# Performance work log

Measured on AMD Instinct MI355X. Metric: run time of the kernel, lower is better.

## Reference

```python
import jax, jax.numpy as jnp
import numpy as np

IN_CHS = 128
NUM_HEADS = 4
WIN = 7
N = WIN * WIN            # 49 tokens per window
QKDIM = 128              # ceil(in_chs/num_groups/num_heads)*num_heads
HEAD_DIM = QKDIM // NUM_HEADS
SCALE = HEAD_DIM ** -0.5
B = 4096                 # batch * num_windows


def _relative_position_index(win_h, win_w):
    coords = np.stack(np.meshgrid(np.arange(win_h), np.arange(win_w), indexing='ij'))  # [2,h,w]
    cf = coords.reshape(2, -1)                      # [2, N]
    rc = (cf[:, :, None] - cf[:, None, :]).transpose(1, 2, 0).astype(np.int64)  # [N,N,2]
    rc[:, :, 0] += win_h - 1
    rc[:, :, 1] += win_w - 1
    rc[:, :, 0] *= 2 * win_w - 1
    return rc.sum(-1)                               # [N, N]


def setup_inputs() -> dict:
    key = jax.random.key(0)
    ks = jax.random.split(key, 8)
    x = jax.random.normal(ks[0], (B, N, IN_CHS), dtype=jnp.float32)
    qk_w = jax.random.normal(ks[1], (2 * QKDIM, IN_CHS), dtype=jnp.float32) * 0.02
    qk_b = jnp.zeros((2 * QKDIM,), dtype=jnp.float32)
    v_w = jax.random.normal(ks[2], (IN_CHS, IN_CHS), dtype=jnp.float32) * 0.02
    v_b = jnp.zeros((IN_CHS,), dtype=jnp.float32)
    proj_w = jax.random.normal(ks[3], (IN_CHS, IN_CHS), dtype=jnp.float32) * 0.02
    proj_b = jnp.zeros((IN_CHS,), dtype=jnp.float32)
    bias_table = jax.random.normal(ks[4], ((2 * WIN - 1) * (2 * WIN - 1), NUM_HEADS), dtype=jnp.float32) * 0.02
    rel_idx = jnp.asarray(_relative_position_index(WIN, WIN))  # [N,N] int64
    return {"x": x, "qk_w": qk_w, "qk_b": qk_b, "v_w": v_w, "v_b": v_b,
            "proj_w": proj_w, "proj_b": proj_b, "bias_table": bias_table,
            "rel_idx": rel_idx}


def reference(x, qk_w, qk_b, v_w, v_b, proj_w, proj_b, bias_table, rel_idx):
    Bn, Nn, C = x.shape
    # fused q/k projection: [B,N,2*qkdim] -> q,k each [B,H,N,d]
    qk = (x @ qk_w.T + qk_b).reshape(Bn, Nn, 2, NUM_HEADS, HEAD_DIM)
    q = qk[:, :, 0].transpose(0, 2, 1, 3)
    k = qk[:, :, 1].transpose(0, 2, 1, 3)
    v = (x @ v_w.T + v_b).reshape(Bn, Nn, NUM_HEADS, -1).transpose(0, 2, 1, 3)
    # windowed QK^T with gathered relative-position bias
    attn = jnp.einsum('bhnd,bhmd->bhnm', q * SCALE, k)
    bias = bias_table[rel_idx.reshape(-1)].reshape(Nn, Nn, NUM_HEADS).transpose(2, 0, 1)
    attn = jax.nn.softmax(attn + bias[None], axis=-1)
    out = jnp.einsum('bhnm,bhmd->bhnd', attn, v).transpose(0, 2, 1, 3).reshape(Bn, Nn, -1)
    return out @ proj_w.T + proj_b
```

## Files before the change

kernel.cpp:

```cpp
#include <hip/hip_runtime.h>
#include <hip/hip_bf16.h>

typedef __attribute__((ext_vector_type(8))) __bf16 bf16x8;
typedef __attribute__((ext_vector_type(4))) float f32x4;

#define MFMA(a,b,c) __builtin_amdgcn_mfma_f32_16x16x32_bf16((a),(b),(c),0,0,0)

#define XB 0u
#define QB 16384u
#define KB 32768u
#define VT 49152u

static __device__ __forceinline__ unsigned short f2u(float x) {
  return __builtin_bit_cast(unsigned short, static_cast<__bf16>(x));
}
static __device__ __forceinline__ unsigned long long pack4(float a, float b, float c, float d) {
  return (unsigned long long)f2u(a) | ((unsigned long long)f2u(b) << 16) |
         ((unsigned long long)f2u(c) << 32) | ((unsigned long long)f2u(d) << 48);
}
static __device__ __forceinline__ unsigned sw256(unsigned row, unsigned colb) {
  return (row << 8) + (colb ^ ((row & 7u) << 4));
}
static __device__ __forceinline__ unsigned sw128(unsigned row, unsigned colb) {
  return (row << 7) + (colb ^ ((row & 7u) << 4));
}

__global__ void rsa_prep(const float* __restrict__ qk_w, const float* __restrict__ v_w,
                         const float* __restrict__ proj_w, const float* __restrict__ bias_table,
                         unsigned short* __restrict__ wqk, unsigned short* __restrict__ wv,
                         unsigned short* __restrict__ wp, float* __restrict__ biasNN) {
  int t = blockIdx.x * blockDim.x + threadIdx.x;
  int stride = gridDim.x * blockDim.x;
  for (int i = t; i < 256 * 128; i += stride) wqk[i] = f2u(qk_w[i]);
  for (int i = t; i < 128 * 128; i += stride) wv[i] = f2u(v_w[i]);
  for (int i = t; i < 128 * 128; i += stride) wp[i] = f2u(proj_w[i]);
  for (int i = t; i < 4 * 64 * 64; i += stride) {
    int h = i >> 12, r = (i >> 6) & 63, m = i & 63;
    float v = -1e9f;
    if (r < 49 && m < 49) {
      int ri = r / 7, rj = r - ri * 7, mi = m / 7, mj = m - mi * 7;
      int rel = (ri - mi + 6) * 13 + (rj - mj + 6);
      v = bias_table[rel * 4 + h];
    }
    biasNN[i] = v;
  }
}

__global__ __launch_bounds__(512, 4) void rsa_main(
    const float* __restrict__ x, const float* __restrict__ qk_bias,
    const float* __restrict__ v_bias, const float* __restrict__ proj_bias,
    const unsigned short* __restrict__ wqk, const unsigned short* __restrict__ wv,
    const unsigned short* __restrict__ wp, const float* __restrict__ biasNN,
    float* __restrict__ out) {
  __shared__ __align__(16) unsigned char LDS[65536];
  const int tid = threadIdx.x;
  const int w = tid >> 6;
  const int lane = tid & 63;
  const int c = lane & 15;
  const int g = lane >> 4;
  const int b = blockIdx.x;
  const float SCALE = 0.17677669529663687f;

  {
    const f32x4* xp = reinterpret_cast<const f32x4*>(x + (size_t)b * 6272);
    for (int i = tid; i < 1568; i += 512) {
      f32x4 v = xp[i];
      unsigned row = (unsigned)i >> 5, c4 = (unsigned)i & 31;
      *reinterpret_cast<unsigned long long*>(LDS + XB + sw256(row, c4 * 8)) =
          pack4(v[0], v[1], v[2], v[3]);
    }
    for (int i = tid; i < 480; i += 512) {
      unsigned row = 49 + ((unsigned)i >> 5), c4 = (unsigned)i & 31;
      *reinterpret_cast<unsigned long long*>(LDS + XB + sw256(row, c4 * 8)) = 0ull;
    }
  }
  __syncthreads();

#pragma unroll
  for (int mi = 0; mi < 2; ++mi) {
    const int mt = w + 8 * mi;
    bf16x8 a[4];
    const unsigned short* wrow = wqk + (mt * 16 + c) * 128 + g * 8;
#pragma unroll
    for (int ks = 0; ks < 4; ++ks) a[ks] = *reinterpret_cast<const bf16x8*>(wrow + ks * 32);
    const int chout = mt * 16 + g * 4;
    f32x4 bias4 = *reinterpret_cast<const f32x4*>(qk_bias + chout);
#pragma unroll
    for (int nt = 0; nt < 4; ++nt) {
      f32x4 acc = {0.f, 0.f, 0.f, 0.f};
#pragma unroll
      for (int ks = 0; ks < 4; ++ks) {
        bf16x8 bf = *reinterpret_cast<const bf16x8*>(LDS + XB + sw256(nt * 16 + c, (ks * 32 + g * 8) * 2));
        acc = MFMA(a[ks], bf, acc);
      }
      const unsigned tok = nt * 16 + c;
      const unsigned colb = ((mt & 7) * 16 + g * 4) * 2;
      float v0 = acc[0] + bias4[0], v1 = acc[1] + bias4[1];
      float v2 = acc[2] + bias4[2], v3 = acc[3] + bias4[3];
      if (mi == 0) { v0 *= SCALE; v1 *= SCALE; v2 *= SCALE; v3 *= SCALE; }
      const unsigned base = (mi == 0) ? QB : KB;
      *reinterpret_cast<unsigned long long*>(LDS + base + sw256(tok, colb)) = pack4(v0, v1, v2, v3);
    }
  }

  {
    const float vb = v_bias[w * 16 + c];
    bf16x8 bw[4];
    const unsigned short* wrow = wv + (w * 16 + c) * 128 + g * 8;
#pragma unroll
    for (int ks = 0; ks < 4; ++ks) bw[ks] = *reinterpret_cast<const bf16x8*>(wrow + ks * 32);
#pragma unroll
    for (int mt = 0; mt < 4; ++mt) {
      f32x4 acc = {0.f, 0.f, 0.f, 0.f};
#pragma unroll
      for (int ks = 0; ks < 4; ++ks) {
        bf16x8 af = *reinterpret_cast<const bf16x8*>(LDS + XB + sw256(mt * 16 + c, (ks * 32 + g * 8) * 2));
        acc = MFMA(af, bw[ks], acc);
      }
      const unsigned row = w * 16 + c;
      const unsigned colb = (mt * 16 + g * 4) * 2;
      *reinterpret_cast<unsigned long long*>(LDS + VT + sw128(row, colb)) =
          pack4(acc[0] + vb, acc[1] + vb, acc[2] + vb, acc[3] + vb);
    }
  }
  __syncthreads();

  const int h = w >> 1;
  const int rt0 = (w & 1) * 2;
  f32x4 s[2][4];
#pragma unroll
  for (int r2 = 0; r2 < 2; ++r2) {
    const int rt = rt0 + r2;
    bf16x8 qf = *reinterpret_cast<const bf16x8*>(LDS + QB + sw256(rt * 16 + c, h * 64 + g * 16));
#pragma unroll
    for (int mt = 0; mt < 4; ++mt) {
      bf16x8 kf = *reinterpret_cast<const bf16x8*>(LDS + KB + sw256(mt * 16 + c, h * 64 + g * 16));
      f32x4 z = {0.f, 0.f, 0.f, 0.f};
      s[r2][mt] = MFMA(kf, qf, z);
    }
  }
  __syncthreads();

#pragma unroll
  for (int r2 = 0; r2 < 2; ++r2) {
    const int r = (rt0 + r2) * 16 + c;
    const float* bp = biasNN + ((h * 64 + r) << 6);
    float v[16];
#pragma unroll
    for (int mt = 0; mt < 4; ++mt) {
      f32x4 bb = *reinterpret_cast<const f32x4*>(bp + mt * 16 + g * 4);
#pragma unroll
      for (int j = 0; j < 4; ++j) v[mt * 4 + j] = s[r2][mt][j] + bb[j];
    }
    float mx = v[0];
#pragma unroll
    for (int j = 1; j < 16; ++j) mx = fmaxf(mx, v[j]);
    mx = fmaxf(mx, __shfl_xor(mx, 16));
    mx = fmaxf(mx, __shfl_xor(mx, 32));
    float sum = 0.f;
#pragma unroll
    for (int j = 0; j < 16; ++j) { v[j] = __expf(v[j] - mx); sum += v[j]; }
    sum += __shfl_xor(sum, 16);
    sum += __shfl_xor(sum, 32);
    const float inv = 1.0f / sum;
#pragma unroll
    for (int mt = 0; mt < 4; ++mt) {
      *reinterpret_cast<unsigned long long*>(LDS + QB + h * 8192 + sw128(r, (mt * 16 + g * 4) * 2)) =
          pack4(v[mt * 4] * inv, v[mt * 4 + 1] * inv, v[mt * 4 + 2] * inv, v[mt * 4 + 3] * inv);
    }
  }

#pragma unroll
  for (int dt = 0; dt < 2; ++dt) {
#pragma unroll
    for (int r2 = 0; r2 < 2; ++r2) {
      const int r = (rt0 + r2) * 16 + c;
      f32x4 acc = {0.f, 0.f, 0.f, 0.f};
#pragma unroll
      for (int ks = 0; ks < 2; ++ks) {
        bf16x8 af = *reinterpret_cast<const bf16x8*>(LDS + VT + sw128(h * 32 + dt * 16 + c, (ks * 32 + g * 8) * 2));
        bf16x8 pf = *reinterpret_cast<const bf16x8*>(LDS + QB + h * 8192 + sw128(r, (ks * 32 + g * 8) * 2));
        acc = MFMA(af, pf, acc);
      }
      const unsigned colb = (h * 32 + dt * 16 + g * 4) * 2;
      *reinterpret_cast<unsigned long long*>(LDS + XB + sw256(r, colb)) =
          pack4(acc[0], acc[1], acc[2], acc[3]);
    }
  }
  __syncthreads();

  {
    bf16x8 ap[4];
    const unsigned short* wrow = wp + (w * 16 + c) * 128 + g * 8;
#pragma unroll
    for (int ks = 0; ks < 4; ++ks) ap[ks] = *reinterpret_cast<const bf16x8*>(wrow + ks * 32);
    f32x4 pb4 = *reinterpret_cast<const f32x4*>(proj_bias + w * 16 + g * 4);
#pragma unroll
    for (int nt = 0; nt < 4; ++nt) {
      f32x4 acc = {0.f, 0.f, 0.f, 0.f};
#pragma unroll
      for (int ks = 0; ks < 4; ++ks) {
        bf16x8 bf = *reinterpret_cast<const bf16x8*>(LDS + XB + sw256(nt * 16 + c, (ks * 32 + g * 8) * 2));
        acc = MFMA(ap[ks], bf, acc);
      }
      const int tok = nt * 16 + c;
      if (tok < 49) {
        f32x4 o = {acc[0] + pb4[0], acc[1] + pb4[1], acc[2] + pb4[2], acc[3] + pb4[3]};
        *reinterpret_cast<f32x4*>(out + ((size_t)b * 49 + tok) * 128 + w * 16 + g * 4) = o;
      }
    }
  }
}

extern "C" void kernel_launch(void* const* d_in, const int* in_sizes, int n_in,
                              void* d_out, int out_size, void* d_ws, size_t ws_size,
                              hipStream_t stream) {
  const float* x          = (const float*)d_in[0];
  const float* qk_w       = (const float*)d_in[1];
  const float* qk_b       = (const float*)d_in[2];
  const float* v_w        = (const float*)d_in[3];
  const float* v_b        = (const float*)d_in[4];
  const float* proj_w     = (const float*)d_in[5];
  const float* proj_b     = (const float*)d_in[6];
  const float* bias_table = (const float*)d_in[7];
  float* out = (float*)d_out;

  unsigned short* wqk = (unsigned short*)d_ws;
  unsigned short* wv  = wqk + 256 * 128;
  unsigned short* wp  = wv + 128 * 128;
  float* biasNN = (float*)((char*)d_ws + 131072);

  const int B = in_sizes[0] / (49 * 128);

  rsa_prep<<<dim3(128), dim3(512), 0, stream>>>(qk_w, v_w, proj_w, bias_table, wqk, wv, wp, biasNN);
  rsa_main<<<dim3(B), dim3(512), 0, stream>>>(x, qk_b, v_b, proj_b, wqk, wv, wp, biasNN, out);
}
```

Before: 126.6 us.

## Process eight windows per block with register-resident weights and x prefetch

Each block now loops over eight windows instead of one. The Q, K and V weight fragments and the biases are loaded into registers once per block. The next window's x tile is prefetched into registers while the current window is being computed. The Q, K and V projections are fused into one loop that shares the x fragments, and the softmax drops the row-max subtraction. This cuts repeated weight loads and block launch overhead, and overlaps global loads with compute. In exchange it raises register pressure under the existing launch bounds, which may cause spills. It also shrinks the grid to 512 blocks, leaving less parallelism to hide latency, and skipping the max subtraction risks overflow for large logits.

After: 213.7 us. +68.8%, slower.

```diff
diff --git a/kernel.cpp b/kernel.cpp
--- a/kernel.cpp
+++ b/kernel.cpp
@@ -10,6 +10,7 @@
 #define QB 16384u
 #define KB 32768u
 #define VT 49152u
+#define NW 8
 
 static __device__ __forceinline__ unsigned short f2u(float x) {
   return __builtin_bit_cast(unsigned short, static_cast<__bf16>(x));
@@ -17,6 +18,9 @@
 static __device__ __forceinline__ unsigned long long pack4(float a, float b, float c, float d) {
   return (unsigned long long)f2u(a) | ((unsigned long long)f2u(b) << 16) |
          ((unsigned long long)f2u(c) << 32) | ((unsigned long long)f2u(d) << 48);
+}
+static __device__ __forceinline__ unsigned long long pack4v(f32x4 v) {
+  return pack4(v[0], v[1], v[2], v[3]);
 }
 static __device__ __forceinline__ unsigned sw256(unsigned row, unsigned colb) {
   return (row << 8) + (colb ^ ((row & 7u) << 4));
@@ -51,164 +55,164 @@
     const float* __restrict__ v_bias, const float* __restrict__ proj_bias,
     const unsigned short* __restrict__ wqk, const unsigned short* __restrict__ wv,
     const unsigned short* __restrict__ wp, const float* __restrict__ biasNN,
-    float* __restrict__ out) {
+    float* __restrict__ out, int Btot) {
   __shared__ __align__(16) unsigned char LDS[65536];
   const int tid = threadIdx.x;
   const int w = tid >> 6;
   const int lane = tid & 63;
   const int c = lane & 15;
   const int g = lane >> 4;
-  const int b = blockIdx.x;
   const float SCALE = 0.17677669529663687f;
 
+  bf16x8 aq[4], ak[4], bv[4];
+  {
+    const unsigned short* rq = wqk + (w * 16 + c) * 128 + g * 8;
+    const unsigned short* rk = wqk + (128 + w * 16 + c) * 128 + g * 8;
+    const unsigned short* rv = wv + (w * 16 + c) * 128 + g * 8;
+#pragma unroll
+    for (int ks = 0; ks < 4; ++ks) {
+      aq[ks] = *reinterpret_cast<const bf16x8*>(rq + ks * 32);
+      ak[ks] = *reinterpret_cast<const bf16x8*>(rk + ks * 32);
+      bv[ks] = *reinterpret_cast<const bf16x8*>(rv + ks * 32);
+    }
+  }
+  const f32x4 qb4 = *reinterpret_cast<const f32x4*>(qk_bias + w * 16 + g * 4);
+  const f32x4 kb4 = *reinterpret_cast<const f32x4*>(qk_bias + 128 + w * 16 + g * 4);
+  const f32x4 pb4 = *reinterpret_cast<const f32x4*>(proj_bias + w * 16 + g * 4);
+  const float vb = v_bias[w * 16 + c];
+  const int h = w >> 1;
+  const int rt0 = (w & 1) * 2;
+
+  int b = blockIdx.x * NW;
+  if (b >= Btot) return;
+  const int nw = (Btot - b < NW) ? (Btot - b) : NW;
+
+  f32x4 xr[4];
   {
     const f32x4* xp = reinterpret_cast<const f32x4*>(x + (size_t)b * 6272);
-    for (int i = tid; i < 1568; i += 512) {
-      f32x4 v = xp[i];
-      unsigned row = (unsigned)i >> 5, c4 = (unsigned)i & 31;
-      *reinterpret_cast<unsigned long long*>(LDS + XB + sw256(row, c4 * 8)) =
-          pack4(v[0], v[1], v[2], v[3]);
-    }
-    for (int i = tid; i < 480; i += 512) {
-      unsigned row = 49 + ((unsigned)i >> 5), c4 = (unsigned)i & 31;
-      *reinterpret_cast<unsigned long long*>(LDS + XB + sw256(row, c4 * 8)) = 0ull;
-    }
-  }
-  __syncthreads();
-
-#pragma unroll
-  for (int mi = 0; mi < 2; ++mi) {
-    const int mt = w + 8 * mi;
-    bf16x8 a[4];
-    const unsigned short* wrow = wqk + (mt * 16 + c) * 128 + g * 8;
-#pragma unroll
-    for (int ks = 0; ks < 4; ++ks) a[ks] = *reinterpret_cast<const bf16x8*>(wrow + ks * 32);
-    const int chout = mt * 16 + g * 4;
-    f32x4 bias4 = *reinterpret_cast<const f32x4*>(qk_bias + chout);
+#pragma unroll
+    for (int j = 0; j < 3; ++j) xr[j] = xp[tid + j * 512];
+    if (tid < 32) xr[3] = xp[tid + 1536];
+    else xr[3] = f32x4{0.f, 0.f, 0.f, 0.f};
+  }
+
+  for (int i = 0; i < nw; ++i) {
+#pragma unroll
+    for (int j = 0; j < 4; ++j) {
+      unsigned idx = (unsigned)tid + (unsigned)j * 512u;
+      unsigned row = idx >> 5, c4 = idx & 31u;
+      *reinterpret_cast<unsigned long long*>(LDS + XB + sw256(row, c4 * 8)) = pack4v(xr[j]);
+    }
+    __syncthreads();
+
+    if (i + 1 < nw) {
+      const f32x4* xp = reinterpret_cast<const f32x4*>(x + (size_t)(b + 1) * 6272);
+#pragma unroll
+      for (int j = 0; j < 3; ++j) xr[j] = xp[tid + j * 512];
+      if (tid < 32) xr[3] = xp[tid + 1536];
+    }
+
 #pragma unroll
     for (int nt = 0; nt < 4; ++nt) {
-      f32x4 acc = {0.f, 0.f, 0.f, 0.f};
+      bf16x8 xf[4];
+#pragma unroll
+      for (int ks = 0; ks < 4; ++ks)
+        xf[ks] = *reinterpret_cast<const bf16x8*>(LDS + XB + sw256(nt * 16 + c, (ks * 32 + g * 8) * 2));
+      f32x4 accq = {0.f, 0.f, 0.f, 0.f}, acck = {0.f, 0.f, 0.f, 0.f}, accv = {0.f, 0.f, 0.f, 0.f};
 #pragma unroll
       for (int ks = 0; ks < 4; ++ks) {
-        bf16x8 bf = *reinterpret_cast<const bf16x8*>(LDS + XB + sw256(nt * 16 + c, (ks * 32 + g * 8) * 2));
-        acc = MFMA(a[ks], bf, acc);
+        accq = MFMA(aq[ks], xf[ks], accq);
+        acck = MFMA(ak[ks], xf[ks], acck);
+        accv = MFMA(xf[ks], bv[ks], accv);
       }
       const unsigned tok = nt * 16 + c;
-      const unsigned colb = ((mt & 7) * 16 + g * 4) * 2;
-      float v0 = acc[0] + bias4[0], v1 = acc[1] + bias4[1];
-      float v2 = acc[2] + bias4[2], v3 = acc[3] + bias4[3];
-      if (mi == 0) { v0 *= SCALE; v1 *= SCALE; v2 *= SCALE; v3 *= SCALE; }
-      const unsigned base = (mi == 0) ? QB : KB;
-      *reinterpret_cast<unsigned long long*>(LDS + base + sw256(tok, colb)) = pack4(v0, v1, v2, v3);
-    }
-  }
-
-  {
-    const float vb = v_bias[w * 16 + c];
-    bf16x8 bw[4];
-    const unsigned short* wrow = wv + (w * 16 + c) * 128 + g * 8;
-#pragma unroll
-    for (int ks = 0; ks < 4; ++ks) bw[ks] = *reinterpret_cast<const bf16x8*>(wrow + ks * 32);
-#pragma unroll
-    for (int mt = 0; mt < 4; ++mt) {
-      f32x4 acc = {0.f, 0.f, 0.f, 0.f};
-#pragma unroll
-      for (int ks = 0; ks < 4; ++ks) {
-        bf16x8 af = *reinterpret_cast<const bf16x8*>(LDS + XB + sw256(mt * 16 + c, (ks * 32 + g * 8) * 2));
-        acc = MFMA(af, bw[ks], acc);
-      }
-      const unsigned row = w * 16 + c;
-      const unsigned colb = (mt * 16 + g * 4) * 2;
-      *reinterpret_cast<unsigned long long*>(LDS + VT + sw128(row, colb)) =
-          pack4(acc[0] + vb, acc[1] + vb, acc[2] + vb, acc[3] + vb);
-    }
-  }
-  __syncthreads();
-
-  const int h = w >> 1;
-  const int rt0 = (w & 1) * 2;
-  f32x4 s[2][4];
-#pragma unroll
-  for (int r2 = 0; r2 < 2; ++r2) {
-    const int rt = rt0 + r2;
-    bf16x8 qf = *reinterpret_cast<const bf16x8*>(LDS + QB + sw256(rt * 16 + c, h * 64 + g * 16));
-#pragma unroll
-    for (int mt = 0; mt < 4; ++mt) {
-      bf16x8 kf = *reinterpret_cast<const bf16x8*>(LDS + KB + sw256(mt * 16 + c, h * 64 + g * 16));
-      f32x4 z = {0.f, 0.f, 0.f, 0.f};
-      s[r2][mt] = MFMA(kf, qf, z);
-    }
-  }
-  __syncthreads();
-
-#pragma unroll
-  for (int r2 = 0; r2 < 2; ++r2) {
-    const int r = (rt0 + r2) * 16 + c;
-    const float* bp = biasNN + ((h * 64 + r) << 6);
-    float v[16];
-#pragma unroll
-    for (int mt = 0; mt < 4; ++mt) {
-      f32x4 bb = *reinterpret_cast<const f32x4*>(bp + mt * 16 + g * 4);
-#pragma unroll
-      for (int j = 0; j < 4; ++j) v[mt * 4 + j] = s[r2][mt][j] + bb[j];
-    }
-    float mx = v[0];
-#pragma unroll
-    for (int j = 1; j < 16; ++j) mx = fmaxf(mx, v[j]);
-    mx = fmaxf(mx, __shfl_xor(mx, 16));
-    mx = fmaxf(mx, __shfl_xor(mx, 32));
-    float sum = 0.f;
-#pragma unroll
-    for (int j = 0; j < 16; ++j) { v[j] = __expf(v[j] - mx); sum += v[j]; }
-    sum += __shfl_xor(sum, 16);
-    sum += __shfl_xor(sum, 32);
-    const float inv = 1.0f / sum;
-#pragma unroll
-    for (int mt = 0; mt < 4; ++mt) {
-      *reinterpret_cast<unsigned long long*>(LDS + QB + h * 8192 + sw128(r, (mt * 16 + g * 4) * 2)) =
-          pack4(v[mt * 4] * inv, v[mt * 4 + 1] * inv, v[mt * 4 + 2] * inv, v[mt * 4 + 3] * inv);
-    }
-  }
-
-#pragma unroll
-  for (int dt = 0; dt < 2; ++dt) {
+      const unsigned cb = (w * 16 + g * 4) * 2;
+      *reinterpret_cast<unsigned long long*>(LDS + QB + sw256(tok, cb)) =
+          pack4((accq[0] + qb4[0]) * SCALE, (accq[1] + qb4[1]) * SCALE,
+                (accq[2] + qb4[2]) * SCALE, (accq[3] + qb4[3]) * SCALE);
+      *reinterpret_cast<unsigned long long*>(LDS + KB + sw256(tok, cb)) =
+          pack4(acck[0] + kb4[0], acck[1] + kb4[1], acck[2] + kb4[2], acck[3] + kb4[3]);
+      *reinterpret_cast<unsigned long long*>(LDS + VT + sw128(w * 16 + c, (nt * 16 + g * 4) * 2)) =
+          pack4(accv[0] + vb, accv[1] + vb, accv[2] + vb, accv[3] + vb);
+    }
+    __syncthreads();
+
+    f32x4 s[2][4];
+#pragma unroll
+    for (int r2 = 0; r2 < 2; ++r2) {
+      bf16x8 qf = *reinterpret_cast<const bf16x8*>(LDS + QB + sw256((rt0 + r2) * 16 + c, h * 64 + g * 16));
+#pragma unroll
+      for (int mt = 0; mt < 4; ++mt) {
+        bf16x8 kf = *reinterpret_cast<const bf16x8*>(LDS + KB + sw256(mt * 16 + c, h * 64 + g * 16));
+        f32x4 z = {0.f, 0.f, 0.f, 0.f};
+        s[r2][mt] = MFMA(kf, qf, z);
+      }
+    }
+    __syncthreads();
+
 #pragma unroll
     for (int r2 = 0; r2 < 2; ++r2) {
       const int r = (rt0 + r2) * 16 + c;
-      f32x4 acc = {0.f, 0.f, 0.f, 0.f};
-#pragma unroll
-      for (int ks = 0; ks < 2; ++ks) {
-        bf16x8 af = *reinterpret_cast<const bf16x8*>(LDS + VT + sw128(h * 32 + dt * 16 + c, (ks * 32 + g * 8) * 2));
-        bf16x8 pf = *reinterpret_cast<const bf16x8*>(LDS + QB + h * 8192 + sw128(r, (ks * 32 + g * 8) * 2));
-        acc = MFMA(af, pf, acc);
-      }
-      const unsigned colb = (h * 32 + dt * 16 + g * 4) * 2;
-      *reinterpret_cast<unsigned long long*>(LDS + XB + sw256(r, colb)) =
-          pack4(acc[0], acc[1], acc[2], acc[3]);
-    }
-  }
-  __syncthreads();
-
-  {
-    bf16x8 ap[4];
-    const unsigned short* wrow = wp + (w * 16 + c) * 128 + g * 8;
-#pragma unroll
-    for (int ks = 0; ks < 4; ++ks) ap[ks] = *reinterpret_cast<const bf16x8*>(wrow + ks * 32);
-    f32x4 pb4 = *reinterpret_cast<const f32x4*>(proj_bias + w * 16 + g * 4);
-#pragma unroll
-    for (int nt = 0; nt < 4; ++nt) {
-      f32x4 acc = {0.f, 0.f, 0.f, 0.f};
-#pragma unroll
-      for (int ks = 0; ks < 4; ++ks) {
-        bf16x8 bf = *reinterpret_cast<const bf16x8*>(LDS + XB + sw256(nt * 16 + c, (ks * 32 + g * 8) * 2));
-        acc = MFMA(ap[ks], bf, acc);
-      }
-      const int tok = nt * 16 + c;
-      if (tok < 49) {
-        f32x4 o = {acc[0] + pb4[0], acc[1] + pb4[1], acc[2] + pb4[2], acc[3] + pb4[3]};
-        *reinterpret_cast<f32x4*>(out + ((size_t)b * 49 + tok) * 128 + w * 16 + g * 4) = o;
-      }
-    }
+      const float* bp = biasNN + ((h * 64 + r) << 6);
+      float v[16];
+      float sum = 0.f;
+#pragma unroll
+      for (int mt = 0; mt < 4; ++mt) {
+        f32x4 bb = *reinterpret_cast<const f32x4*>(bp + mt * 16 + g * 4);
+#pragma unroll
+        for (int j = 0; j < 4; ++j) {
+          v[mt * 4 + j] = __expf(s[r2][mt][j] + bb[j]);
+          sum += v[mt * 4 + j];
+        }
+      }
+      sum += __shfl_xor(sum, 16);
+      sum += __shfl_xor(sum, 32);
+      const float inv = (sum > 0.f) ? 1.0f / sum : 0.f;
+#pragma unroll
+      for (int mt = 0; mt < 4; ++mt)
+        *reinterpret_cast<unsigned long long*>(LDS + QB + h * 8192 + sw128(r, (mt * 16 + g * 4) * 2)) =
+            pack4(v[mt * 4] * inv, v[mt * 4 + 1] * inv, v[mt * 4 + 2] * inv, v[mt * 4 + 3] * inv);
+    }
+
+#pragma unroll
+    for (int dt = 0; dt < 2; ++dt) {
+#pragma unroll
+      for (int r2 = 0; r2 < 2; ++r2) {
+        const int r = (rt0 + r2) * 16 + c;
+        f32x4 acc = {0.f, 0.f, 0.f, 0.f};
+#pragma unroll
+        for (int ks = 0; ks < 2; ++ks) {
+          bf16x8 af = *reinterpret_cast<const bf16x8*>(LDS + VT + sw128(h * 32 + dt * 16 + c, (ks * 32 + g * 8) * 2));
+          bf16x8 pf = *reinterpret_cast<const bf16x8*>(LDS + QB + h * 8192 + sw128(r, (ks * 32 + g * 8) * 2));
+          acc = MFMA(af, pf, acc);
+        }
+        *reinterpret_cast<unsigned long long*>(LDS + XB + sw256(r, (h * 32 + dt * 16 + g * 4) * 2)) = pack4v(acc);
+      }
+    }
+    __syncthreads();
+
+    {
+      bf16x8 apf[4];
+      const unsigned short* rp = wp + (w * 16 + c) * 128 + g * 8;
+#pragma unroll
+      for (int ks = 0; ks < 4; ++ks) apf[ks] = *reinterpret_cast<const bf16x8*>(rp + ks * 32);
+#pragma unroll
+      for (int nt = 0; nt < 4; ++nt) {
+        f32x4 acc = {0.f, 0.f, 0.f, 0.f};
+#pragma unroll
+        for (int ks = 0; ks < 4; ++ks) {
+          bf16x8 bf = *reinterpret_cast<const bf16x8*>(LDS + XB + sw256(nt * 16 + c, (ks * 32 + g * 8) * 2));
+          acc = MFMA(apf[ks], bf, acc);
+        }
+        const int tok = nt * 16 + c;
+        if (tok < 49) {
+          f32x4 o = {acc[0] + pb4[0], acc[1] + pb4[1], acc[2] + pb4[2], acc[3] + pb4[3]};
+          *reinterpret_cast<f32x4*>(out + ((size_t)b * 49 + tok) * 128 + w * 16 + g * 4) = o;
+        }
+      }
+    }
+    __syncthreads();
+    ++b;
   }
 }
 
@@ -231,7 +235,8 @@
   float* biasNN = (float*)((char*)d_ws + 131072);
 
   const int B = in_sizes[0] / (49 * 128);
+  const int grid = (B + NW - 1) / NW;
 
   rsa_prep<<<dim3(128), dim3(512), 0, stream>>>(qk_w, v_w, proj_w, bias_table, wqk, wv, wp, biasNN);
-  rsa_main<<<dim3(B), dim3(512), 0, stream>>>(x, qk_b, v_b, proj_b, wqk, wv, wp, biasNN, out);
-}
+  rsa_main<<<dim3(grid), dim3(512), 0, stream>>>(x, qk_b, v_b, proj_b, wqk, wv, wp, biasNN, out, B);
+}
```
